# Optimization experiments

Hardware: AMD Instinct MI355X
Metric: run time of the kernel (lower is better)

## Reference

```python
import math
import jax, jax.numpy as jnp
import numpy as np

BETA = 6.0
LOG_2PI = math.log(2.0 * math.pi)


def setup_inputs() -> dict:
    key = jax.random.key(0)
    k1, k2, k3, k4 = jax.random.split(key, 4)
    B, D = 2048, 64
    return {
        "kl": jax.random.uniform(k1, (B, D), dtype=jnp.float32),
        "z_mean": jax.random.normal(k2, (B, D), dtype=jnp.float32),
        "z_logvar": jax.random.normal(k3, (B, D), dtype=jnp.float32),
        "z_sampled": jax.random.normal(k4, (B, D), dtype=jnp.float32),
    }


def _gaussian_log_density(samples, mean, log_var):
    # samples: [B,1,D], mean/log_var: [1,B,D] -> [B,B,D]
    inv_sigma = jnp.exp(-log_var)
    tmp = samples - mean
    return -0.5 * (tmp * tmp * inv_sigma + log_var + LOG_2PI)


def _total_correlation(z, z_mean, z_logvar):
    # [B, B, D] pairwise per-dimension log q(z_i | x_j)
    log_qz_prob = _gaussian_log_density(z[:, None, :], z_mean[None, :, :], z_logvar[None, :, :])
    # log prod_l q(z_l): logsumexp over batch per dim, then sum over dims
    log_qz_product = jnp.sum(jax.nn.logsumexp(log_qz_prob, axis=1), axis=1)  # [B]
    # log q(z): sum over dims first, then logsumexp over batch
    log_qz = jax.nn.logsumexp(jnp.sum(log_qz_prob, axis=2), axis=1)  # [B]
    return jnp.mean(log_qz - log_qz_product)


def reference(kl, z_mean, z_logvar, z_sampled):
    kl_loss = jnp.sum(kl)
    tc = (BETA - 1.0) * _total_correlation(z_sampled, z_mean, z_logvar)
    return tc + kl_loss
```

## Files before the change

kernel.cpp:

```cpp
#include <hip/hip_runtime.h>
#include <math.h>

#define B 2048
#define D 64
#define G 256
#define NCH 32
#define NC2 16
#define NBLK 2048

#define ZLO (-5.5f)
#define DZ  (11.0f / 255.0f)
#define INVDZ (255.0f / 11.0f)

typedef float v2f  __attribute__((ext_vector_type(2)));
typedef short bf16x8 __attribute__((ext_vector_type(8)));
typedef float f32x4  __attribute__((ext_vector_type(4)));

static __device__ __forceinline__ float exp2fast(float x) { return __builtin_amdgcn_exp2f(x); }
static __device__ __forceinline__ float log2fast(float x) { return __builtin_amdgcn_logf(x); }
static __device__ __forceinline__ unsigned short f2bf(float x) {
    unsigned u = __float_as_uint(x);
    u += 0x7fff + ((u >> 16) & 1);
    return (unsigned short)(u >> 16);
}

__global__ __launch_bounds__(256) void k_pre(
    const float* __restrict__ kl, const float* __restrict__ zm,
    const float* __restrict__ zlv, const float* __restrict__ zs,
    uint2* __restrict__ packhg, unsigned short* __restrict__ Zx,
    unsigned short* __restrict__ Wt, float* __restrict__ QQ,
    float* __restrict__ klp, float* __restrict__ out)
{
    const float LOG2E   = 1.4426950408889634f;
    const float LOG_2PI = 1.8378770664093453f;
    __shared__ float red[4];
    int wv = threadIdx.x >> 6, d = threadIdx.x & 63;
    int j = blockIdx.x * 4 + wv;
    int idx = j * D + d;
    float lv = zlv[idx];
    float mu = zm[idx];
    float zz = zs[idx];
    float is = exp2fast(-LOG2E * lv);
    float h  = -0.5f * LOG2E * is;
    float cv = -0.5f * LOG2E * (lv + LOG_2PI);
    float g  = -2.0f * mu * h;
    float q  = fmaf(mu * mu, h, cv);
    packhg[idx] = make_uint2(((unsigned)f2bf(h) << 16) | f2bf(g),
                             __float_as_uint(q));
    Wt[j * 128 + d]      = f2bf(h);
    Wt[j * 128 + 64 + d] = f2bf(g);
    Zx[j * 128 + d]      = f2bf(zz * zz);
    Zx[j * 128 + 64 + d] = f2bf(zz);

    float qs = q, ks = kl[idx];
#pragma unroll
    for (int off = 32; off; off >>= 1) {
        qs += __shfl_xor(qs, off);
        ks += __shfl_xor(ks, off);
    }
    if (d == 0) { QQ[j] = qs; red[wv] = ks; }
    __syncthreads();
    if (threadIdx.x == 0) {
        klp[blockIdx.x] = red[0] + red[1] + red[2] + red[3];
        if (blockIdx.x == 0) out[0] = 0.0f;
    }
}

static __device__ __forceinline__ void role_lse(
    int lw, const unsigned short* __restrict__ Zx,
    const unsigned short* __restrict__ Wt, const float* __restrict__ QQ,
    float* __restrict__ wsM, float* __restrict__ wsL)
{
    int lane  = threadIdx.x & 63;
    int i0    = (lw >> 4) * 16;
    int chunk = lw & 15;
    int jbase = chunk * 128;
    int r16 = lane & 15, kg = lane >> 4;

    const bf16x8* Za = (const bf16x8*)(Zx + (size_t)(i0 + r16) * 128 + kg * 8);
    bf16x8 a[4];
#pragma unroll
    for (int s = 0; s < 4; ++s) a[s] = Za[s * 4];

    float m[4], l[4];
#pragma unroll
    for (int r = 0; r < 4; ++r) { m[r] = -3.0e38f; l[r] = 0.0f; }

    for (int t = 0; t < 8; ++t) {
        int j = jbase + t * 16 + r16;
        const bf16x8* Wb = (const bf16x8*)(Wt + (size_t)j * 128 + kg * 8);
        f32x4 c = (f32x4){0.0f, 0.0f, 0.0f, 0.0f};
#pragma unroll
        for (int s = 0; s < 4; ++s)
            c = __builtin_amdgcn_mfma_f32_16x16x32_bf16(a[s], Wb[s * 4], c, 0, 0, 0);
        float qq = QQ[j];
#pragma unroll
        for (int r = 0; r < 4; ++r) {
            float val = c[r] + qq;
            float delta = val - m[r];
            float e = exp2fast(-fabsf(delta));
            l[r] = (delta <= 0.0f) ? (l[r] + e) : fmaf(l[r], e, 1.0f);
            m[r] = fmaxf(m[r], val);
        }
    }
#pragma unroll
    for (int off = 8; off; off >>= 1) {
#pragma unroll
        for (int r = 0; r < 4; ++r) {
            float m2 = __shfl_xor(m[r], off);
            float l2 = __shfl_xor(l[r], off);
            float M  = fmaxf(m[r], m2);
            l[r] = fmaf(l[r], exp2fast(m[r] - M), l2 * exp2fast(m2 - M));
            m[r] = M;
        }
    }
    if (r16 == 0) {
#pragma unroll
        for (int r = 0; r < 4; ++r) {
            int i = i0 + kg * 4 + r;
            wsM[i * NC2 + chunk] = m[r];
            wsL[i * NC2 + chunk] = l[r];
        }
    }
}

__global__ __launch_bounds__(256) void k_mega(
    const uint2* __restrict__ packhg, float* __restrict__ accS,
    const unsigned short* __restrict__ Zx, const unsigned short* __restrict__ Wt,
    const float* __restrict__ QQ, float* __restrict__ wsM, float* __restrict__ wsL)
{
    __shared__ float lds[4][4 * 64];
    int tid  = threadIdx.x;
    int wv   = tid >> 6, lane = tid & 63;
    int bid  = blockIdx.x;
    int chunk = bid & (NCH - 1);
    int t0    = (bid >> 5) * 4;
    int j0    = chunk * 64 + wv * 16;

    v2f zt[2], zt2[2], ap[2];
#pragma unroll
    for (int kp = 0; kp < 2; ++kp) {
        float za = ZLO + (float)(t0 + 2 * kp) * DZ;
        float zb = ZLO + (float)(t0 + 2 * kp + 1) * DZ;
        zt[kp]  = (v2f){za, zb};
        zt2[kp] = (v2f){za * za, zb * zb};
        ap[kp]  = (v2f){0.0f, 0.0f};
    }

#pragma unroll 4
    for (int j = j0; j < j0 + 16; ++j) {
        uint2 p = packhg[j * D + lane];
        float h = __uint_as_float(p.x & 0xFFFF0000u);
        float g = __uint_as_float(p.x << 16);
        float q = __uint_as_float(p.y);
        v2f hh = (v2f){h, h};
        v2f gg = (v2f){g, g};
        v2f qq = (v2f){q, q};
#pragma unroll
        for (int kp = 0; kp < 2; ++kp) {
            v2f arg = zt2[kp] * hh + (zt[kp] * gg + qq);
            v2f e;
            e.x = exp2fast(arg.x);
            e.y = exp2fast(arg.y);
            ap[kp] += e;
        }
    }

#pragma unroll
    for (int kp = 0; kp < 2; ++kp) {
        lds[wv][(2 * kp) * 64 + lane]     = ap[kp].x;
        lds[wv][(2 * kp + 1) * 64 + lane] = ap[kp].y;
    }
    __syncthreads();
    accS[(size_t)chunk * G * D + (size_t)t0 * D + tid] =
        lds[0][tid] + lds[1][tid] + lds[2][tid] + lds[3][tid];

    if (wv == 0)
        role_lse(bid, Zx, Wt, QQ, wsM, wsL);
}

__global__ __launch_bounds__(256) void k_tab(
    const float* __restrict__ accS, float* __restrict__ T)
{
    int e = blockIdx.x * 256 + threadIdx.x;
    float s = 0.0f;
#pragma unroll
    for (int c = 0; c < NCH; ++c)
        s += accS[(size_t)c * G * D + e];
    T[e] = log2fast(s);
}

__global__ __launch_bounds__(256) void k_fin(
    const float* __restrict__ z, const float* __restrict__ T,
    const float* __restrict__ wsM, const float* __restrict__ wsL,
    const float* __restrict__ klp, float* __restrict__ out)
{
    const float LN2 = 0.6931471805599453f;
    __shared__ float red[4];
    int lane = threadIdx.x & 63;
    int wv   = threadIdx.x >> 6;
    int i    = blockIdx.x * 4 + wv;

    float zv = z[i * D + lane];
    float tf = (zv - ZLO) * INVDZ;
    int   it = (int)floorf(tf);
    it = min(max(it, 1), G - 3);
    float u = tf - (float)it;
    float y0 = T[(it - 1) * D + lane];
    float y1 = T[it * D + lane];
    float y2 = T[(it + 1) * D + lane];
    float y3 = T[(it + 2) * D + lane];
    float ca = fmaf(1.5f, y1 - y2, 0.5f * (y3 - y0));
    float cb = y0 - 2.5f * y1 + 2.0f * y2 - 0.5f * y3;
    float cc = 0.5f * (y2 - y0);
    float lqp2 = fmaf(fmaf(fmaf(ca, u, cb), u, cc), u, y1);
#pragma unroll
    for (int off = 32; off; off >>= 1) lqp2 += __shfl_xor(lqp2, off);

    float m = -3.0e38f, l = 0.0f;
    if (lane < NC2) { m = wsM[i * NC2 + lane]; l = wsL[i * NC2 + lane]; }
#pragma unroll
    for (int off = 32; off; off >>= 1) {
        float m2 = __shfl_xor(m, off);
        float l2 = __shfl_xor(l, off);
        float M  = fmaxf(m, m2);
        l = fmaf(l, exp2fast(m - M), l2 * exp2fast(m2 - M));
        m = M;
    }

    if (lane == 0)
        red[wv] = (m + log2fast(l) - lqp2) * LN2;
    __syncthreads();
    if (threadIdx.x == 0)
        atomicAdd(out, (red[0] + red[1] + red[2] + red[3]) * (5.0f / 2048.0f)
                       + klp[blockIdx.x]);
}

extern "C" void kernel_launch(void* const* d_in, const int* in_sizes, int n_in,
                              void* d_out, int out_size, void* d_ws, size_t ws_size,
                              hipStream_t stream)
{
    const float* kl  = (const float*)d_in[0];
    const float* zm  = (const float*)d_in[1];
    const float* zlv = (const float*)d_in[2];
    const float* zs  = (const float*)d_in[3];
    float* out = (float*)d_out;
    float* ws  = (float*)d_ws;

    uint2*          packhg = (uint2*)ws;
    unsigned short* Zx   = (unsigned short*)(ws + 2 * B * D);
    unsigned short* Wt   = (unsigned short*)(ws + 3 * B * D);
    float*          QQ   = ws + 4 * B * D;
    float*          wsM  = QQ + B;
    float*          wsL  = wsM + (size_t)B * NC2;
    float*          accS = wsL + (size_t)B * NC2;
    float*          T    = accS + (size_t)NCH * G * D;
    float*          klp  = T + (size_t)G * D;

    k_pre<<<B / 4, 256, 0, stream>>>(kl, zm, zlv, zs, packhg, Zx, Wt, QQ, klp, out);
    k_mega<<<NBLK, 256, 0, stream>>>(packhg, accS, Zx, Wt, QQ, wsM, wsL);
    k_tab<<<(G * D) / 256, 256, 0, stream>>>(accS, T);
    k_fin<<<B / 4, 256, 0, stream>>>(zs, T, wsM, wsL, klp, out);
}
```

Before: 37.56 us.

## Replace partial-sum table and reduction kernel with atomic accumulation

The separate table-reduction kernel is removed. Waves in the main kernel now atomically add their per-grid-point exp sums straight into one zeroed accumulator, and the final kernel takes log2 of the accumulator on the fly. Work is also rebalanced: wave 0 runs only the logsumexp MFMA role, and the other three waves split the 2048 j-rows into 96 slices per grid group. This saves one kernel launch and the 32-way partial buffer traffic, in exchange for many float atomics on the same addresses (contention) and a summation order that is no longer deterministic.

```diff
diff --git a/kernel.cpp b/kernel.cpp
--- a/kernel.cpp
+++ b/kernel.cpp
@@ -4,9 +4,9 @@
 #define B 2048
 #define D 64
 #define G 256
-#define NCH 32
 #define NC2 16
 #define NBLK 2048
+#define NSL 96
 
 #define ZLO (-5.5f)
 #define DZ  (11.0f / 255.0f)
@@ -29,7 +29,7 @@
     const float* __restrict__ zlv, const float* __restrict__ zs,
     uint2* __restrict__ packhg, unsigned short* __restrict__ Zx,
     unsigned short* __restrict__ Wt, float* __restrict__ QQ,
-    float* __restrict__ klp, float* __restrict__ out)
+    float* __restrict__ klp, float* __restrict__ acc, float* __restrict__ out)
 {
     const float LOG2E   = 1.4426950408889634f;
     const float LOG_2PI = 1.8378770664093453f;
@@ -37,6 +37,8 @@
     int wv = threadIdx.x >> 6, d = threadIdx.x & 63;
     int j = blockIdx.x * 4 + wv;
     int idx = j * D + d;
+    if (blockIdx.x < (G * D) / 256)
+        acc[blockIdx.x * 256 + threadIdx.x] = 0.0f;
     float lv = zlv[idx];
     float mu = zm[idx];
     float zz = zs[idx];
@@ -125,17 +127,25 @@
 }
 
 __global__ __launch_bounds__(256) void k_mega(
-    const uint2* __restrict__ packhg, float* __restrict__ accS,
+    const uint2* __restrict__ packhg, float* __restrict__ acc,
     const unsigned short* __restrict__ Zx, const unsigned short* __restrict__ Wt,
     const float* __restrict__ QQ, float* __restrict__ wsM, float* __restrict__ wsL)
 {
-    __shared__ float lds[4][4 * 64];
     int tid  = threadIdx.x;
     int wv   = tid >> 6, lane = tid & 63;
     int bid  = blockIdx.x;
-    int chunk = bid & (NCH - 1);
-    int t0    = (bid >> 5) * 4;
-    int j0    = chunk * 64 + wv * 16;
+
+    if (wv == 0) {
+        role_lse(bid, Zx, Wt, QQ, wsM, wsL);
+        return;
+    }
+
+    int w     = bid * 3 + (wv - 1);
+    int tg    = w / 96;
+    int slice = w - tg * 96;
+    int t0    = tg * 4;
+    int nj    = 21 + (slice < 32 ? 1 : 0);
+    int j0    = slice * 21 + min(slice, 32);
 
     v2f zt[2], zt2[2], ap[2];
 #pragma unroll
@@ -148,7 +158,7 @@
     }
 
 #pragma unroll 4
-    for (int j = j0; j < j0 + 16; ++j) {
+    for (int j = j0; j < j0 + nj; ++j) {
         uint2 p = packhg[j * D + lane];
         float h = __uint_as_float(p.x & 0xFFFF0000u);
         float g = __uint_as_float(p.x << 16);
@@ -168,30 +178,13 @@
 
 #pragma unroll
     for (int kp = 0; kp < 2; ++kp) {
-        lds[wv][(2 * kp) * 64 + lane]     = ap[kp].x;
-        lds[wv][(2 * kp + 1) * 64 + lane] = ap[kp].y;
-    }
-    __syncthreads();
-    accS[(size_t)chunk * G * D + (size_t)t0 * D + tid] =
-        lds[0][tid] + lds[1][tid] + lds[2][tid] + lds[3][tid];
-
-    if (wv == 0)
-        role_lse(bid, Zx, Wt, QQ, wsM, wsL);
-}
-
-__global__ __launch_bounds__(256) void k_tab(
-    const float* __restrict__ accS, float* __restrict__ T)
-{
-    int e = blockIdx.x * 256 + threadIdx.x;
-    float s = 0.0f;
-#pragma unroll
-    for (int c = 0; c < NCH; ++c)
-        s += accS[(size_t)c * G * D + e];
-    T[e] = log2fast(s);
+        atomicAdd(&acc[(t0 + 2 * kp) * D + lane],     ap[kp].x);
+        atomicAdd(&acc[(t0 + 2 * kp + 1) * D + lane], ap[kp].y);
+    }
 }
 
 __global__ __launch_bounds__(256) void k_fin(
-    const float* __restrict__ z, const float* __restrict__ T,
+    const float* __restrict__ z, const float* __restrict__ acc,
     const float* __restrict__ wsM, const float* __restrict__ wsL,
     const float* __restrict__ klp, float* __restrict__ out)
 {
@@ -206,10 +199,10 @@
     int   it = (int)floorf(tf);
     it = min(max(it, 1), G - 3);
     float u = tf - (float)it;
-    float y0 = T[(it - 1) * D + lane];
-    float y1 = T[it * D + lane];
-    float y2 = T[(it + 1) * D + lane];
-    float y3 = T[(it + 2) * D + lane];
+    float y0 = log2fast(acc[(it - 1) * D + lane]);
+    float y1 = log2fast(acc[it * D + lane]);
+    float y2 = log2fast(acc[(it + 1) * D + lane]);
+    float y3 = log2fast(acc[(it + 2) * D + lane]);
     float ca = fmaf(1.5f, y1 - y2, 0.5f * (y3 - y0));
     float cb = y0 - 2.5f * y1 + 2.0f * y2 - 0.5f * y3;
     float cc = 0.5f * (y2 - y0);
@@ -253,12 +246,10 @@
     float*          QQ   = ws + 4 * B * D;
     float*          wsM  = QQ + B;
     float*          wsL  = wsM + (size_t)B * NC2;
-    float*          accS = wsL + (size_t)B * NC2;
-    float*          T    = accS + (size_t)NCH * G * D;
-    float*          klp  = T + (size_t)G * D;
-
-    k_pre<<<B / 4, 256, 0, stream>>>(kl, zm, zlv, zs, packhg, Zx, Wt, QQ, klp, out);
-    k_mega<<<NBLK, 256, 0, stream>>>(packhg, accS, Zx, Wt, QQ, wsM, wsL);
-    k_tab<<<(G * D) / 256, 256, 0, stream>>>(accS, T);
-    k_fin<<<B / 4, 256, 0, stream>>>(zs, T, wsM, wsL, klp, out);
-}
+    float*          acc  = wsL + (size_t)B * NC2;
+    float*          klp  = acc + (size_t)G * D;
+
+    k_pre<<<B / 4, 256, 0, stream>>>(kl, zm, zlv, zs, packhg, Zx, Wt, QQ, klp, acc, out);
+    k_mega<<<NBLK, 256, 0, stream>>>(packhg, acc, Zx, Wt, QQ, wsM, wsL);
+    k_fin<<<B / 4, 256, 0, stream>>>(zs, acc, wsM, wsL, klp, out);
+}
```

New measurement: 37.34 us. Within noise of the previous version (-0.6%).
